# Kernel optimization log

Measured on AMD Instinct MI355X. Metric: run time of the kernel, lower is better.

Reference implementation:

```python
import jax, jax.numpy as jnp
import numpy as np

N = 10000
E = 640000
IN_CH = 512
OUT_CH = 256
K = 2


def setup_inputs() -> dict:
    key = jax.random.key(0)
    k1, k2, k3, k4, k5 = jax.random.split(key, 5)
    x = jax.random.normal(k1, (N, IN_CH), dtype=jnp.float32)
    edge_index = jax.random.randint(k2, (2, E), 0, N, dtype=jnp.int64)
    lin_w = jax.random.normal(k3, (OUT_CH, IN_CH), dtype=jnp.float32) * (1.0 / np.sqrt(IN_CH))
    lin_b = jax.random.normal(k4, (OUT_CH,), dtype=jnp.float32) * 0.01
    weights = jax.random.uniform(k5, (K,), dtype=jnp.float32)
    return {"x": x, "edge_index": edge_index, "lin_w": lin_w, "lin_b": lin_b, "weights": weights}


def reference(x, edge_index, lin_w, lin_b, weights):
    n = x.shape[0]
    row, col = edge_index[0], edge_index[1]
    # deg = bincount(row); symmetric-normalized edge weights
    deg = jax.ops.segment_sum(jnp.ones(row.shape[0], dtype=x.dtype), row, num_segments=n)
    deg_inv_sqrt = jnp.where(deg > 0, jax.lax.rsqrt(deg), 0.0)
    norm = deg_inv_sqrt[row] * deg_inv_sqrt[col]  # [E]

    def spmm(h):
        # y[i] = sum_{e: row[e]==i} norm[e] * h[col[e]]
        return jax.ops.segment_sum(norm[:, None] * h[col], row, num_segments=n)

    out = x @ lin_w.T + lin_b  # [N, OUT_CH]
    # Faithful ARMA loop: x_k starts from the CURRENT accumulated `out` each hop-group
    for k in range(K):
        x_k = out
        for _ in range(k + 1):
            x_k = spmm(x_k)
        out = out + weights[k] * x_k
    return out
```

## Files before the change

### kernel.cpp

```cpp
#include <hip/hip_runtime.h>

#define N_NODES 10000
#define E_EDGES 640000
#define IN_CH   512
#define OUT_CH  256
#define HALF_CH 128
#define CSR_CAP (E_EDGES + 16 * N_NODES + 128)
#define G_GEMM_X 157
#define G_GEMM  (G_GEMM_X * 2)
#define HBLK    125
#define EPB     5120
#define G_SCALE 2500
#define G_CONVX 2500
#define G_CONVW 64
#define G_ALLOCA 2500

typedef short bf16x8 __attribute__((ext_vector_type(8)));
typedef float f32x4  __attribute__((ext_vector_type(4)));

__device__ __forceinline__ unsigned short f2b(float f) {
    unsigned int u = __float_as_uint(f);
    return (unsigned short)((u + 0x7FFFu + ((u >> 16) & 1u)) >> 16);
}
__device__ __forceinline__ float lo16(unsigned int u) { return __uint_as_float(u << 16); }
__device__ __forceinline__ float hi16(unsigned int u) { return __uint_as_float(u & 0xFFFF0000u); }
__device__ __forceinline__ float b2f(unsigned short u) { return __uint_as_float(((unsigned int)u) << 16); }

__global__ __launch_bounds__(256) void conv_hist(const float* __restrict__ x,
                                                 const float* __restrict__ w,
                                                 unsigned short* __restrict__ xb,
                                                 unsigned short* __restrict__ wb,
                                                 const int* __restrict__ row,
                                                 int* __restrict__ cnt,
                                                 unsigned short* __restrict__ rank) {
    int bid = blockIdx.x;
    int tid = threadIdx.x;
    if (bid < HBLK) {
        __shared__ int hist[N_NODES];
        for (int i = tid; i < N_NODES; i += 256) hist[i] = 0;
        __syncthreads();
        int ebase = bid * EPB;
        for (int i = tid; i < EPB; i += 256) {
            int r = row[ebase + i];
            rank[ebase + i] = (unsigned short)atomicAdd(&hist[r], 1);
        }
        __syncthreads();
        int* cb = cnt + (size_t)bid * N_NODES;
        for (int i = tid; i < N_NODES; i += 256) cb[i] = hist[i];
        return;
    }
    int u = bid - HBLK;
    const float* src;
    unsigned short* dst;
    size_t base;
    if (u < G_CONVX) { src = x;  dst = xb; base = (size_t)u * 2048 + tid * 8; }
    else             { src = w;  dst = wb; base = (size_t)(u - G_CONVX) * 2048 + tid * 8; }
    float4 a = *(const float4*)(src + base);
    float4 b = *(const float4*)(src + base + 4);
    ushort4 lo, hi;
    lo.x = f2b(a.x); lo.y = f2b(a.y); lo.z = f2b(a.z); lo.w = f2b(a.w);
    hi.x = f2b(b.x); hi.y = f2b(b.y); hi.z = f2b(b.z); hi.w = f2b(b.w);
    *(ushort4*)(dst + base) = lo;
    *(ushort4*)(dst + base + 4) = hi;
}

__global__ __launch_bounds__(256) void gemm_alloca(const unsigned short* __restrict__ xb,
                                                   const unsigned short* __restrict__ wb,
                                                   const float* __restrict__ bias,
                                                   float* __restrict__ h0f,
                                                   int* __restrict__ cnt,
                                                   int2* __restrict__ pd,
                                                   float* __restrict__ dinv, float* __restrict__ sq,
                                                   int* __restrict__ pads, int n) {
    __shared__ unsigned short As[64][72];
    __shared__ unsigned short Bs[128][72];
    int bid = blockIdx.x;
    int tid = threadIdx.x;
    if (bid >= G_GEMM) {
        int r = (bid - G_GEMM) * 4 + (tid >> 6);
        int lane = tid & 63;
        if (r >= n) return;
        int v0 = cnt[(size_t)lane * N_NODES + r];
        int v1 = (lane < HBLK - 64) ? cnt[(size_t)(64 + lane) * N_NODES + r] : 0;
        int s0 = v0, s1 = v1;
        #pragma unroll
        for (int off = 1; off < 64; off <<= 1) {
            int t0 = __shfl_up(s0, off, 64);
            int t1 = __shfl_up(s1, off, 64);
            if (lane >= off) { s0 += t0; s1 += t1; }
        }
        int tot0 = __shfl(s0, 63, 64);
        int d = tot0 + __shfl(s1, 63, 64);
        int pad = (d + 15) & ~15;
        cnt[(size_t)lane * N_NODES + r] = s0 - v0;
        if (lane < HBLK - 64) cnt[(size_t)(64 + lane) * N_NODES + r] = tot0 + s1 - v1;
        if (lane == 0) {
            dinv[r] = (d > 0) ? rsqrtf((float)d) : 0.0f;
            sq[r]   = (d > 0) ? sqrtf((float)d) : 0.0f;
            pd[r] = make_int2(d, pad);
            pads[r] = pad;
        }
        return;
    }
    int bx = bid % G_GEMM_X;
    int plane = bid / G_GEMM_X;
    int wave = tid >> 6, lane = tid & 63, quad = lane >> 4, l16 = lane & 15;
    int row0 = bx * 64;
    int n0 = plane * 128;
    float* h0f_p = h0f + (size_t)plane * N_NODES * HALF_CH;

    int ar = tid >> 2;
    int aseg = (tid & 3) * 16;
    int br = tid >> 1;
    int bseg = (tid & 1) * 32;

    f32x4 acc[8] = {};
    for (int k0 = 0; k0 < IN_CH; k0 += 64) {
        {
            int gr = row0 + ar;
            if (gr < N_NODES) {
                const uint4* src = (const uint4*)(xb + (size_t)gr * IN_CH + k0 + aseg);
                *(uint4*)&As[ar][aseg]     = src[0];
                *(uint4*)&As[ar][aseg + 8] = src[1];
            } else {
                uint4 z = {0, 0, 0, 0};
                *(uint4*)&As[ar][aseg]     = z;
                *(uint4*)&As[ar][aseg + 8] = z;
            }
        }
        {
            const uint4* src = (const uint4*)(wb + (size_t)(n0 + br) * IN_CH + k0 + bseg);
            *(uint4*)&Bs[br][bseg]      = src[0];
            *(uint4*)&Bs[br][bseg + 8]  = src[1];
            *(uint4*)&Bs[br][bseg + 16] = src[2];
            *(uint4*)&Bs[br][bseg + 24] = src[3];
        }
        __syncthreads();
        #pragma unroll
        for (int kk = 0; kk < 2; kk++) {
            bf16x8 a = *(const bf16x8*)&As[wave * 16 + l16][kk * 32 + quad * 8];
            #pragma unroll
            for (int t = 0; t < 8; t++) {
                bf16x8 b = *(const bf16x8*)&Bs[t * 16 + l16][kk * 32 + quad * 8];
                acc[t] = __builtin_amdgcn_mfma_f32_16x16x32_bf16(a, b, acc[t], 0, 0, 0);
            }
        }
        __syncthreads();
    }
    #pragma unroll
    for (int t = 0; t < 8; t++) {
        int lcol = t * 16 + l16;
        float bv = bias[n0 + lcol];
        #pragma unroll
        for (int r = 0; r < 4; r++) {
            int grow = row0 + wave * 16 + quad * 4 + r;
            if (grow < N_NODES)
                h0f_p[(size_t)grow * HALF_CH + lcol] = acc[t][r] + bv;
        }
    }
}

__global__ __launch_bounds__(1024) void scan_pads(const int* __restrict__ pads,
                                                  int* __restrict__ rowstart, int n) {
    __shared__ int ls[1024];
    int t = threadIdx.x;
    int base = t * 10;
    int loc[10];
    int sum = 0;
    if (base < n) {
        #pragma unroll
        for (int i = 0; i < 10; i++) { loc[i] = pads[base + i]; sum += loc[i]; }
    }
    ls[t] = sum;
    __syncthreads();
    for (int off = 1; off < 1024; off <<= 1) {
        int v = (t >= off) ? ls[t - off] : 0;
        __syncthreads();
        ls[t] += v;
        __syncthreads();
    }
    if (base < n) {
        int run = ls[t] - sum;
        #pragma unroll
        for (int i = 0; i < 10; i++) { rowstart[base + i] = run; run += loc[i]; }
    }
}

__global__ __launch_bounds__(256) void alloc_b(const int* __restrict__ rowstart,
                                               const int2* __restrict__ pd,
                                               int2* __restrict__ seg,
                                               unsigned short* __restrict__ csr_col, int n) {
    int r = blockIdx.x * 4 + (threadIdx.x >> 6);
    int lane = threadIdx.x & 63;
    if (r >= n) return;
    int s = rowstart[r];
    int2 pd_ = pd[r];
    if (lane == 0) seg[r] = make_int2(s, s + pd_.y);
    int j = pd_.x + lane;
    if (j < pd_.y) csr_col[s + j] = (unsigned short)N_NODES;
}

__global__ __launch_bounds__(256) void scatter_scale(const int* __restrict__ row,
                                                     const int* __restrict__ col,
                                                     const int* __restrict__ base,
                                                     const int* __restrict__ rowstart,
                                                     const unsigned short* __restrict__ rank,
                                                     unsigned short* __restrict__ csr_col,
                                                     const float* __restrict__ h0f,
                                                     const float* __restrict__ dinv,
                                                     unsigned short* __restrict__ h0b) {
    int bid = blockIdx.x;
    int tid = threadIdx.x;
    size_t pstride = (size_t)(N_NODES + 1) * HALF_CH;
    if (bid < HBLK) {
        __shared__ int bs[N_NODES];
        const int4* cb4 = (const int4*)(base + (size_t)bid * N_NODES);
        const int4* rs4 = (const int4*)rowstart;
        for (int i = tid; i < N_NODES / 4; i += 256) {
            int4 c = cb4[i];
            int4 r = rs4[i];
            int4 o;
            o.x = c.x + r.x; o.y = c.y + r.y; o.z = c.z + r.z; o.w = c.w + r.w;
            ((int4*)bs)[i] = o;
        }
        __syncthreads();
        int ebase = bid * EPB;
        for (int i = tid; i < EPB; i += 256) {
            int e = ebase + i;
            int p = bs[row[e]] + (int)rank[e];
            csr_col[p] = (unsigned short)col[e];
        }
        return;
    }
    int idx = bid - HBLK;
    int node = idx * 4 + (tid >> 6);
    int lane = tid & 63;
    float di = dinv[node];
    #pragma unroll
    for (int plane = 0; plane < 2; plane++) {
        const float2* src = (const float2*)(h0f + (size_t)plane * N_NODES * HALF_CH
                                            + (size_t)node * HALF_CH);
        float2 v = src[lane];
        unsigned int o = (unsigned int)f2b(v.x * di) | ((unsigned int)f2b(v.y * di) << 16);
        ((unsigned int*)(h0b + (size_t)plane * pstride + (size_t)node * HALF_CH))[lane] = o;
    }
    if (idx == 0 && tid < 128) {
        int plane = tid >> 6;
        ((unsigned int*)(h0b + (size_t)plane * pstride + (size_t)N_NODES * HALF_CH))[tid & 63] = 0u;
    }
}

__global__ __launch_bounds__(256) void spmm_kernel(const unsigned short* __restrict__ hb,
                                                   const int2* __restrict__ seg,
                                                   const unsigned short* __restrict__ csr_col,
                                                   const float* __restrict__ dinv,
                                                   const float* __restrict__ sq,
                                                   const unsigned short* __restrict__ prev_b,
                                                   const float* __restrict__ wts, int widx,
                                                   unsigned short* __restrict__ yb_out,
                                                   float* __restrict__ axpy_out,
                                                   unsigned short* __restrict__ axpyb_out,
                                                   int n) {
    int plane = blockIdx.x & 1;
    int node = (blockIdx.x >> 1) * 4 + (threadIdx.x >> 6);
    int lane = threadIdx.x & 63;
    if (node >= n) return;
    int sub = lane >> 4, l16 = lane & 15;
    size_t pstride = (size_t)(n + 1) * HALF_CH;
    const unsigned short* hp = hb + (size_t)plane * pstride;

    int2 se = seg[node];
    int s = se.x, e = se.y;
    float acc[8] = {0.f, 0.f, 0.f, 0.f, 0.f, 0.f, 0.f, 0.f};
    if (s < e) {
        int cA0 = csr_col[s + 0  + sub];
        int cA1 = csr_col[s + 4  + sub];
        int cA2 = csr_col[s + 8  + sub];
        int cA3 = csr_col[s + 12 + sub];
        uint4 vA0 = *(const uint4*)(hp + (size_t)cA0 * HALF_CH + l16 * 8);
        uint4 vA1 = *(const uint4*)(hp + (size_t)cA1 * HALF_CH + l16 * 8);
        uint4 vA2 = *(const uint4*)(hp + (size_t)cA2 * HALF_CH + l16 * 8);
        uint4 vA3 = *(const uint4*)(hp + (size_t)cA3 * HALF_CH + l16 * 8);
        int cB0 = csr_col[s + 16 + sub];
        int cB1 = csr_col[s + 20 + sub];
        int cB2 = csr_col[s + 24 + sub];
        int cB3 = csr_col[s + 28 + sub];
        int p = s;
        while (p + 16 < e) {
            uint4 vB0 = *(const uint4*)(hp + (size_t)cB0 * HALF_CH + l16 * 8);
            uint4 vB1 = *(const uint4*)(hp + (size_t)cB1 * HALF_CH + l16 * 8);
            uint4 vB2 = *(const uint4*)(hp + (size_t)cB2 * HALF_CH + l16 * 8);
            uint4 vB3 = *(const uint4*)(hp + (size_t)cB3 * HALF_CH + l16 * 8);
            int pn = p + 32;
            int cC0 = csr_col[pn + 0  + sub];
            int cC1 = csr_col[pn + 4  + sub];
            int cC2 = csr_col[pn + 8  + sub];
            int cC3 = csr_col[pn + 12 + sub];
            acc[0] += lo16(vA0.x) + lo16(vA1.x) + lo16(vA2.x) + lo16(vA3.x);
            acc[1] += hi16(vA0.x) + hi16(vA1.x) + hi16(vA2.x) + hi16(vA3.x);
            acc[2] += lo16(vA0.y) + lo16(vA1.y) + lo16(vA2.y) + lo16(vA3.y);
            acc[3] += hi16(vA0.y) + hi16(vA1.y) + hi16(vA2.y) + hi16(vA3.y);
            acc[4] += lo16(vA0.z) + lo16(vA1.z) + lo16(vA2.z) + lo16(vA3.z);
            acc[5] += hi16(vA0.z) + hi16(vA1.z) + hi16(vA2.z) + hi16(vA3.z);
            acc[6] += lo16(vA0.w) + lo16(vA1.w) + lo16(vA2.w) + lo16(vA3.w);
            acc[7] += hi16(vA0.w) + hi16(vA1.w) + hi16(vA2.w) + hi16(vA3.w);
            vA0 = vB0; vA1 = vB1; vA2 = vB2; vA3 = vB3;
            cB0 = cC0; cB1 = cC1; cB2 = cC2; cB3 = cC3;
            p += 16;
        }
        acc[0] += lo16(vA0.x) + lo16(vA1.x) + lo16(vA2.x) + lo16(vA3.x);
        acc[1] += hi16(vA0.x) + hi16(vA1.x) + hi16(vA2.x) + hi16(vA3.x);
        acc[2] += lo16(vA0.y) + lo16(vA1.y) + lo16(vA2.y) + lo16(vA3.y);
        acc[3] += hi16(vA0.y) + hi16(vA1.y) + hi16(vA2.y) + hi16(vA3.y);
        acc[4] += lo16(vA0.z) + lo16(vA1.z) + lo16(vA2.z) + lo16(vA3.z);
        acc[5] += hi16(vA0.z) + hi16(vA1.z) + hi16(vA2.z) + hi16(vA3.z);
        acc[6] += lo16(vA0.w) + lo16(vA1.w) + lo16(vA2.w) + lo16(vA3.w);
        acc[7] += hi16(vA0.w) + hi16(vA1.w) + hi16(vA2.w) + hi16(vA3.w);
    }
    #pragma unroll
    for (int k = 0; k < 8; k++) {
        acc[k] += __shfl_xor(acc[k], 16, 64);
        acc[k] += __shfl_xor(acc[k], 32, 64);
    }
    if (sub != 0) return;

    float di = dinv[node];
    float y[8];
    #pragma unroll
    for (int k = 0; k < 8; k++) y[k] = di * acc[k];

    size_t pbase = (size_t)plane * pstride + (size_t)node * HALF_CH + l16 * 8;
    size_t padrow = (size_t)plane * pstride + (size_t)n * HALF_CH + l16 * 8;
    if (yb_out) {
        ushort4 o0, o1;
        o0.x = f2b(di * y[0]); o0.y = f2b(di * y[1]); o0.z = f2b(di * y[2]); o0.w = f2b(di * y[3]);
        o1.x = f2b(di * y[4]); o1.y = f2b(di * y[5]); o1.z = f2b(di * y[6]); o1.w = f2b(di * y[7]);
        *(ushort4*)(yb_out + pbase) = o0;
        *(ushort4*)(yb_out + pbase + 4) = o1;
        if (node == 0) {
            ushort4 z = {0, 0, 0, 0};
            *(ushort4*)(yb_out + padrow) = z;
            *(ushort4*)(yb_out + padrow + 4) = z;
        }
    }
    if (prev_b) {
        float wk = wts[widx];
        float sqn = sq[node];
        ushort4 p0 = *(const ushort4*)(prev_b + pbase);
        ushort4 p1 = *(const ushort4*)(prev_b + pbase + 4);
        float o[8];
        o[0] = b2f(p0.x) * sqn + wk * y[0];
        o[1] = b2f(p0.y) * sqn + wk * y[1];
        o[2] = b2f(p0.z) * sqn + wk * y[2];
        o[3] = b2f(p0.w) * sqn + wk * y[3];
        o[4] = b2f(p1.x) * sqn + wk * y[4];
        o[5] = b2f(p1.y) * sqn + wk * y[5];
        o[6] = b2f(p1.z) * sqn + wk * y[6];
        o[7] = b2f(p1.w) * sqn + wk * y[7];
        if (axpy_out) {
            size_t fbase = (size_t)node * OUT_CH + plane * HALF_CH + l16 * 8;
            float4 f0 = {o[0], o[1], o[2], o[3]};
            float4 f1 = {o[4], o[5], o[6], o[7]};
            *(float4*)(axpy_out + fbase) = f0;
            *(float4*)(axpy_out + fbase + 4) = f1;
        }
        if (axpyb_out) {
            ushort4 b0, b1;
            b0.x = f2b(di * o[0]); b0.y = f2b(di * o[1]); b0.z = f2b(di * o[2]); b0.w = f2b(di * o[3]);
            b1.x = f2b(di * o[4]); b1.y = f2b(di * o[5]); b1.z = f2b(di * o[6]); b1.w = f2b(di * o[7]);
            *(ushort4*)(axpyb_out + pbase) = b0;
            *(ushort4*)(axpyb_out + pbase + 4) = b1;
            if (node == 0) {
                ushort4 z = {0, 0, 0, 0};
                *(ushort4*)(axpyb_out + padrow) = z;
                *(ushort4*)(axpyb_out + padrow + 4) = z;
            }
        }
    }
}

extern "C" void kernel_launch(void* const* d_in, const int* in_sizes, int n_in,
                              void* d_out, int out_size, void* d_ws, size_t ws_size,
                              hipStream_t stream) {
    const float* x     = (const float*)d_in[0];
    const int*   ei    = (const int*)d_in[1];
    const float* lin_w = (const float*)d_in[2];
    const float* lin_b = (const float*)d_in[3];
    const float* wts   = (const float*)d_in[4];
    float* out = (float*)d_out;

    char* ws = (char*)d_ws;
    size_t off = 0;
    auto alloc = [&](size_t bytes) -> void* {
        void* p = ws + off;
        off += (bytes + 255) & ~(size_t)255;
        return p;
    };
    int*   cnt      = (int*)  alloc((size_t)HBLK * N_NODES * 4);
    unsigned short* rank = (unsigned short*)alloc((size_t)E_EDGES * 2);
    int2*  pd       = (int2*) alloc((size_t)N_NODES * 8);
    int*   pads     = (int*)  alloc((size_t)N_NODES * 4);
    int*   rowstart = (int*)  alloc((size_t)N_NODES * 4);
    int2*  seg      = (int2*) alloc((size_t)N_NODES * 8);
    float* dinv     = (float*)alloc(N_NODES * 4);
    float* sq       = (float*)alloc(N_NODES * 4);
    unsigned short* csr_col = (unsigned short*)alloc((size_t)CSR_CAP * 2);
    unsigned short* xb = (unsigned short*)alloc((size_t)N_NODES * IN_CH * 2);
    unsigned short* wb = (unsigned short*)alloc((size_t)OUT_CH * IN_CH * 2);
    float* h0f      = (float*)alloc((size_t)2 * N_NODES * HALF_CH * 4);
    unsigned short* h0b   = (unsigned short*)alloc((size_t)2 * (N_NODES + 1) * HALF_CH * 2);
    unsigned short* out1b = (unsigned short*)alloc((size_t)2 * (N_NODES + 1) * HALF_CH * 2);
    unsigned short* t2b   = (unsigned short*)alloc((size_t)2 * (N_NODES + 1) * HALF_CH * 2);

    const int* row = ei;
    const int* col = ei + E_EDGES;

    conv_hist<<<HBLK + G_CONVX + G_CONVW, 256, 0, stream>>>(x, lin_w, xb, wb,
                                                            row, cnt, rank);
    gemm_alloca<<<G_GEMM + G_ALLOCA, 256, 0, stream>>>(xb, wb, lin_b, h0f, cnt,
                                                       pd, dinv, sq, pads, N_NODES);
    scan_pads<<<1, 1024, 0, stream>>>(pads, rowstart, N_NODES);
    alloc_b<<<(N_NODES + 3) / 4, 256, 0, stream>>>(rowstart, pd, seg, csr_col, N_NODES);

    scatter_scale<<<HBLK + G_SCALE, 256, 0, stream>>>(row, col, cnt, rowstart, rank,
                                                      csr_col, h0f, dinv, h0b);

    int sgrid = 2 * ((N_NODES + 3) / 4);
    spmm_kernel<<<sgrid, 256, 0, stream>>>(h0b, seg, csr_col, dinv, sq, h0b,
                                           wts, 0, nullptr, nullptr, out1b, N_NODES);
    spmm_kernel<<<sgrid, 256, 0, stream>>>(out1b, seg, csr_col, dinv, sq, nullptr,
                                           wts, 0, t2b, nullptr, nullptr, N_NODES);
    spmm_kernel<<<sgrid, 256, 0, stream>>>(t2b, seg, csr_col, dinv, sq, out1b,
                                           wts, 1, nullptr, out, nullptr, N_NODES);
}
```

Before: 193.3 us.

## Fuse GEMM epilogue scaling with CSR scatter and padding into one kernel

Moves the per-node degree prefix computation into a small thread-per-node kernel that runs before the GEMM, so dinv is ready when the GEMM finishes. The GEMM epilogue then scales by dinv and writes bf16 directly. This removes the fp32 h0f intermediate and its separate conversion pass. The CSR scatter and pad/segment setup run as extra blocks of the same launch, cutting two launches. The trade-off is that the GEMM now waits behind the alloc and scan kernels instead of overlapping the degree scan, and the serial per-thread scan over 125 histogram rows uses fewer threads.

```diff
diff --git a/kernel.cpp b/kernel.cpp
--- a/kernel.cpp
+++ b/kernel.cpp
@@ -10,10 +10,9 @@
 #define G_GEMM  (G_GEMM_X * 2)
 #define HBLK    125
 #define EPB     5120
-#define G_SCALE 2500
 #define G_CONVX 2500
 #define G_CONVW 64
-#define G_ALLOCA 2500
+#define G_AB    40
 
 typedef short bf16x8 __attribute__((ext_vector_type(8)));
 typedef float f32x4  __attribute__((ext_vector_type(4)));
@@ -64,50 +63,118 @@
     *(ushort4*)(dst + base + 4) = hi;
 }
 
-__global__ __launch_bounds__(256) void gemm_alloca(const unsigned short* __restrict__ xb,
-                                                   const unsigned short* __restrict__ wb,
-                                                   const float* __restrict__ bias,
-                                                   float* __restrict__ h0f,
-                                                   int* __restrict__ cnt,
-                                                   int2* __restrict__ pd,
-                                                   float* __restrict__ dinv, float* __restrict__ sq,
-                                                   int* __restrict__ pads, int n) {
-    __shared__ unsigned short As[64][72];
-    __shared__ unsigned short Bs[128][72];
+__global__ __launch_bounds__(256) void alloc_a2(int* __restrict__ cnt,
+                                                int2* __restrict__ pd,
+                                                float* __restrict__ dinv, float* __restrict__ sq,
+                                                int* __restrict__ pads, int n) {
+    int r = blockIdx.x * 256 + threadIdx.x;
+    if (r >= n) return;
+    int run = 0;
+    int b0 = 0;
+    for (; b0 + 8 <= HBLK; b0 += 8) {
+        int c[8];
+        #pragma unroll
+        for (int j = 0; j < 8; j++) c[j] = cnt[(size_t)(b0 + j) * N_NODES + r];
+        #pragma unroll
+        for (int j = 0; j < 8; j++) {
+            cnt[(size_t)(b0 + j) * N_NODES + r] = run;
+            run += c[j];
+        }
+    }
+    for (; b0 < HBLK; b0++) {
+        int c = cnt[(size_t)b0 * N_NODES + r];
+        cnt[(size_t)b0 * N_NODES + r] = run;
+        run += c;
+    }
+    int d = run;
+    int pad = (d + 15) & ~15;
+    dinv[r] = (d > 0) ? rsqrtf((float)d) : 0.0f;
+    sq[r]   = (d > 0) ? sqrtf((float)d) : 0.0f;
+    pd[r] = make_int2(d, pad);
+    pads[r] = pad;
+}
+
+__global__ __launch_bounds__(1024) void scan_pads(const int* __restrict__ pads,
+                                                  int* __restrict__ rowstart, int n) {
+    __shared__ int ls[1024];
+    int t = threadIdx.x;
+    int base = t * 10;
+    int loc[10];
+    int sum = 0;
+    if (base < n) {
+        #pragma unroll
+        for (int i = 0; i < 10; i++) { loc[i] = pads[base + i]; sum += loc[i]; }
+    }
+    ls[t] = sum;
+    __syncthreads();
+    for (int off = 1; off < 1024; off <<= 1) {
+        int v = (t >= off) ? ls[t - off] : 0;
+        __syncthreads();
+        ls[t] += v;
+        __syncthreads();
+    }
+    if (base < n) {
+        int run = ls[t] - sum;
+        #pragma unroll
+        for (int i = 0; i < 10; i++) { rowstart[base + i] = run; run += loc[i]; }
+    }
+}
+
+__global__ __launch_bounds__(256) void gemm_scatter_ab(const unsigned short* __restrict__ xb,
+                                                       const unsigned short* __restrict__ wb,
+                                                       const float* __restrict__ bias,
+                                                       const float* __restrict__ dinv,
+                                                       unsigned short* __restrict__ h0b,
+                                                       const int* __restrict__ row,
+                                                       const int* __restrict__ col,
+                                                       const int* __restrict__ base,
+                                                       const int* __restrict__ rowstart,
+                                                       const unsigned short* __restrict__ rank,
+                                                       unsigned short* __restrict__ csr_col,
+                                                       const int2* __restrict__ pd,
+                                                       int2* __restrict__ seg) {
+    __shared__ __align__(16) char smem[40960];
     int bid = blockIdx.x;
     int tid = threadIdx.x;
+    if (bid >= G_GEMM + HBLK) {
+        int r = (bid - G_GEMM - HBLK) * 256 + tid;
+        if (r >= N_NODES) return;
+        int s = rowstart[r];
+        int2 pd_ = pd[r];
+        seg[r] = make_int2(s, s + pd_.y);
+        for (int j = pd_.x; j < pd_.y; j++) csr_col[s + j] = (unsigned short)N_NODES;
+        return;
+    }
     if (bid >= G_GEMM) {
-        int r = (bid - G_GEMM) * 4 + (tid >> 6);
-        int lane = tid & 63;
-        if (r >= n) return;
-        int v0 = cnt[(size_t)lane * N_NODES + r];
-        int v1 = (lane < HBLK - 64) ? cnt[(size_t)(64 + lane) * N_NODES + r] : 0;
-        int s0 = v0, s1 = v1;
-        #pragma unroll
-        for (int off = 1; off < 64; off <<= 1) {
-            int t0 = __shfl_up(s0, off, 64);
-            int t1 = __shfl_up(s1, off, 64);
-            if (lane >= off) { s0 += t0; s1 += t1; }
-        }
-        int tot0 = __shfl(s0, 63, 64);
-        int d = tot0 + __shfl(s1, 63, 64);
-        int pad = (d + 15) & ~15;
-        cnt[(size_t)lane * N_NODES + r] = s0 - v0;
-        if (lane < HBLK - 64) cnt[(size_t)(64 + lane) * N_NODES + r] = tot0 + s1 - v1;
-        if (lane == 0) {
-            dinv[r] = (d > 0) ? rsqrtf((float)d) : 0.0f;
-            sq[r]   = (d > 0) ? sqrtf((float)d) : 0.0f;
-            pd[r] = make_int2(d, pad);
-            pads[r] = pad;
+        int sb = bid - G_GEMM;
+        int* bs = (int*)smem;
+        const int4* cb4 = (const int4*)(base + (size_t)sb * N_NODES);
+        const int4* rs4 = (const int4*)rowstart;
+        for (int i = tid; i < N_NODES / 4; i += 256) {
+            int4 c = cb4[i];
+            int4 r = rs4[i];
+            int4 o;
+            o.x = c.x + r.x; o.y = c.y + r.y; o.z = c.z + r.z; o.w = c.w + r.w;
+            ((int4*)bs)[i] = o;
+        }
+        __syncthreads();
+        int ebase = sb * EPB;
+        for (int i = tid; i < EPB; i += 256) {
+            int e = ebase + i;
+            int p = bs[row[e]] + (int)rank[e];
+            csr_col[p] = (unsigned short)col[e];
         }
         return;
     }
+    typedef unsigned short us72[72];
+    us72* As = (us72*)smem;
+    us72* Bs = (us72*)(smem + 64 * 72 * 2);
     int bx = bid % G_GEMM_X;
     int plane = bid / G_GEMM_X;
     int wave = tid >> 6, lane = tid & 63, quad = lane >> 4, l16 = lane & 15;
     int row0 = bx * 64;
     int n0 = plane * 128;
-    float* h0f_p = h0f + (size_t)plane * N_NODES * HALF_CH;
+    unsigned short* h0b_p = h0b + (size_t)plane * (N_NODES + 1) * HALF_CH;
 
     int ar = tid >> 2;
     int aseg = (tid & 3) * 16;
@@ -154,100 +221,14 @@
         #pragma unroll
         for (int r = 0; r < 4; r++) {
             int grow = row0 + wave * 16 + quad * 4 + r;
-            if (grow < N_NODES)
-                h0f_p[(size_t)grow * HALF_CH + lcol] = acc[t][r] + bv;
-        }
-    }
-}
-
-__global__ __launch_bounds__(1024) void scan_pads(const int* __restrict__ pads,
-                                                  int* __restrict__ rowstart, int n) {
-    __shared__ int ls[1024];
-    int t = threadIdx.x;
-    int base = t * 10;
-    int loc[10];
-    int sum = 0;
-    if (base < n) {
-        #pragma unroll
-        for (int i = 0; i < 10; i++) { loc[i] = pads[base + i]; sum += loc[i]; }
-    }
-    ls[t] = sum;
-    __syncthreads();
-    for (int off = 1; off < 1024; off <<= 1) {
-        int v = (t >= off) ? ls[t - off] : 0;
-        __syncthreads();
-        ls[t] += v;
-        __syncthreads();
-    }
-    if (base < n) {
-        int run = ls[t] - sum;
-        #pragma unroll
-        for (int i = 0; i < 10; i++) { rowstart[base + i] = run; run += loc[i]; }
-    }
-}
-
-__global__ __launch_bounds__(256) void alloc_b(const int* __restrict__ rowstart,
-                                               const int2* __restrict__ pd,
-                                               int2* __restrict__ seg,
-                                               unsigned short* __restrict__ csr_col, int n) {
-    int r = blockIdx.x * 4 + (threadIdx.x >> 6);
-    int lane = threadIdx.x & 63;
-    if (r >= n) return;
-    int s = rowstart[r];
-    int2 pd_ = pd[r];
-    if (lane == 0) seg[r] = make_int2(s, s + pd_.y);
-    int j = pd_.x + lane;
-    if (j < pd_.y) csr_col[s + j] = (unsigned short)N_NODES;
-}
-
-__global__ __launch_bounds__(256) void scatter_scale(const int* __restrict__ row,
-                                                     const int* __restrict__ col,
-                                                     const int* __restrict__ base,
-                                                     const int* __restrict__ rowstart,
-                                                     const unsigned short* __restrict__ rank,
-                                                     unsigned short* __restrict__ csr_col,
-                                                     const float* __restrict__ h0f,
-                                                     const float* __restrict__ dinv,
-                                                     unsigned short* __restrict__ h0b) {
-    int bid = blockIdx.x;
-    int tid = threadIdx.x;
-    size_t pstride = (size_t)(N_NODES + 1) * HALF_CH;
-    if (bid < HBLK) {
-        __shared__ int bs[N_NODES];
-        const int4* cb4 = (const int4*)(base + (size_t)bid * N_NODES);
-        const int4* rs4 = (const int4*)rowstart;
-        for (int i = tid; i < N_NODES / 4; i += 256) {
-            int4 c = cb4[i];
-            int4 r = rs4[i];
-            int4 o;
-            o.x = c.x + r.x; o.y = c.y + r.y; o.z = c.z + r.z; o.w = c.w + r.w;
-            ((int4*)bs)[i] = o;
-        }
-        __syncthreads();
-        int ebase = bid * EPB;
-        for (int i = tid; i < EPB; i += 256) {
-            int e = ebase + i;
-            int p = bs[row[e]] + (int)rank[e];
-            csr_col[p] = (unsigned short)col[e];
-        }
-        return;
-    }
-    int idx = bid - HBLK;
-    int node = idx * 4 + (tid >> 6);
-    int lane = tid & 63;
-    float di = dinv[node];
-    #pragma unroll
-    for (int plane = 0; plane < 2; plane++) {
-        const float2* src = (const float2*)(h0f + (size_t)plane * N_NODES * HALF_CH
-                                            + (size_t)node * HALF_CH);
-        float2 v = src[lane];
-        unsigned int o = (unsigned int)f2b(v.x * di) | ((unsigned int)f2b(v.y * di) << 16);
-        ((unsigned int*)(h0b + (size_t)plane * pstride + (size_t)node * HALF_CH))[lane] = o;
-    }
-    if (idx == 0 && tid < 128) {
-        int plane = tid >> 6;
-        ((unsigned int*)(h0b + (size_t)plane * pstride + (size_t)N_NODES * HALF_CH))[tid & 63] = 0u;
-    }
+            if (grow < N_NODES) {
+                float v = acc[t][r] + bv;
+                h0b_p[(size_t)grow * HALF_CH + lcol] = f2b(v * dinv[grow]);
+            }
+        }
+    }
+    if (bx == 0 && tid < 64)
+        ((unsigned int*)(h0b_p + (size_t)N_NODES * HALF_CH))[tid] = 0u;
 }
 
 __global__ __launch_bounds__(256) void spmm_kernel(const unsigned short* __restrict__ hb,
@@ -407,7 +388,6 @@
     unsigned short* csr_col = (unsigned short*)alloc((size_t)CSR_CAP * 2);
     unsigned short* xb = (unsigned short*)alloc((size_t)N_NODES * IN_CH * 2);
     unsigned short* wb = (unsigned short*)alloc((size_t)OUT_CH * IN_CH * 2);
-    float* h0f      = (float*)alloc((size_t)2 * N_NODES * HALF_CH * 4);
     unsigned short* h0b   = (unsigned short*)alloc((size_t)2 * (N_NODES + 1) * HALF_CH * 2);
     unsigned short* out1b = (unsigned short*)alloc((size_t)2 * (N_NODES + 1) * HALF_CH * 2);
     unsigned short* t2b   = (unsigned short*)alloc((size_t)2 * (N_NODES + 1) * HALF_CH * 2);
@@ -417,13 +397,11 @@
 
     conv_hist<<<HBLK + G_CONVX + G_CONVW, 256, 0, stream>>>(x, lin_w, xb, wb,
                                                             row, cnt, rank);
-    gemm_alloca<<<G_GEMM + G_ALLOCA, 256, 0, stream>>>(xb, wb, lin_b, h0f, cnt,
-                                                       pd, dinv, sq, pads, N_NODES);
+    alloc_a2<<<(N_NODES + 255) / 256, 256, 0, stream>>>(cnt, pd, dinv, sq, pads, N_NODES);
     scan_pads<<<1, 1024, 0, stream>>>(pads, rowstart, N_NODES);
-    alloc_b<<<(N_NODES + 3) / 4, 256, 0, stream>>>(rowstart, pd, seg, csr_col, N_NODES);
-
-    scatter_scale<<<HBLK + G_SCALE, 256, 0, stream>>>(row, col, cnt, rowstart, rank,
-                                                      csr_col, h0f, dinv, h0b);
+    gemm_scatter_ab<<<G_GEMM + HBLK + G_AB, 256, 0, stream>>>(xb, wb, lin_b, dinv, h0b,
+                                                              row, col, cnt, rowstart,
+                                                              rank, csr_col, pd, seg);
 
     int sgrid = 2 * ((N_NODES + 3) / 4);
     spmm_kernel<<<sgrid, 256, 0, stream>>>(h0b, seg, csr_col, dinv, sq, h0b,
```

After: 179.3 us. 1.08x faster.
